# Kernel tuning notes

Hardware: AMD Instinct MI355X
Metric: run time of the kernel (lower is better)

Reference implementation:

```python
import jax, jax.numpy as jnp
import numpy as np

B, T, D = 4, 2048, 768
H = 12
DH = D // H
DFF = 3072
EPS = 1e-5


def _layernorm(x, g, b):
    mu = jnp.mean(x, axis=-1, keepdims=True)
    var = jnp.var(x, axis=-1, keepdims=True)
    return (x - mu) * jax.lax.rsqrt(var + EPS) * g + b


def setup_inputs() -> dict:
    key = jax.random.key(0)
    ks = jax.random.split(key, 12)
    s = lambda fan_in: 1.0 / np.sqrt(fan_in)
    return {
        "x": jax.random.normal(ks[0], (B, T, D), dtype=jnp.float32),
        "ln1_g": jnp.ones((D,), jnp.float32),
        "ln1_b": jnp.zeros((D,), jnp.float32),
        "w_qkv": jax.random.uniform(ks[1], (D, 3 * D), jnp.float32, -s(D), s(D)),
        "b_qkv": jax.random.uniform(ks[2], (3 * D,), jnp.float32, -s(D), s(D)),
        "w_proj": jax.random.uniform(ks[3], (D, D), jnp.float32, -s(D), s(D)),
        "b_proj": jax.random.uniform(ks[4], (D,), jnp.float32, -s(D), s(D)),
        "ln2_g": jnp.ones((D,), jnp.float32),
        "ln2_b": jnp.zeros((D,), jnp.float32),
        "w_ff1": jax.random.uniform(ks[5], (D, DFF), jnp.float32, -s(D), s(D)),
        "b_ff1": jax.random.uniform(ks[6], (DFF,), jnp.float32, -s(D), s(D)),
        "w_ff2": jax.random.uniform(ks[7], (DFF, D), jnp.float32, -s(DFF), s(DFF)),
        "b_ff2": jax.random.uniform(ks[8], (D,), jnp.float32, -s(DFF), s(DFF)),
    }


def reference(x, ln1_g, ln1_b, w_qkv, b_qkv, w_proj, b_proj,
              ln2_g, ln2_b, w_ff1, b_ff1, w_ff2, b_ff2):
    # --- attention sublayer ---
    h = _layernorm(x, ln1_g, ln1_b)
    qkv = h @ w_qkv + b_qkv                       # [B,T,3D]
    q, k, v = jnp.split(qkv, 3, axis=-1)
    q = q.reshape(B, T, H, DH).transpose(0, 2, 1, 3)  # [B,H,T,DH]
    k = k.reshape(B, T, H, DH).transpose(0, 2, 1, 3)
    v = v.reshape(B, T, H, DH).transpose(0, 2, 1, 3)
    att = jnp.einsum('bhqd,bhkd->bhqk', q, k) / jnp.sqrt(jnp.float32(DH))
    causal = jnp.tril(jnp.ones((T, T), dtype=bool))
    att = jnp.where(causal, att, -jnp.inf)
    att = jax.nn.softmax(att, axis=-1)
    out = jnp.einsum('bhqk,bhkd->bhqd', att, v)    # [B,H,T,DH]
    out = out.transpose(0, 2, 1, 3).reshape(B, T, D)
    x = x + out @ w_proj + b_proj
    # --- MLP sublayer ---
    h2 = _layernorm(x, ln2_g, ln2_b)
    h2 = jax.nn.gelu(h2 @ w_ff1 + b_ff1, approximate=False)
    x = x + h2 @ w_ff2 + b_ff2
    return x
```

## Files before the change

### kernel.cpp

```cpp
#include <hip/hip_runtime.h>
#include <cstdint>
#include <cstddef>

typedef unsigned short u16;
typedef unsigned int u32;
typedef __attribute__((ext_vector_type(8))) short s16x8;
typedef __attribute__((ext_vector_type(4))) float f32x4;

#define NB 4
#define NT 2048
#define ND 768
#define NH 12
#define NDH 64
#define NFF 3072
#define NM (NB*NT)

__device__ __forceinline__ u16 f2b(float f){
  union { float f; unsigned u; } c; c.f = f;
  unsigned r = c.u + 0x7fffu + ((c.u >> 16) & 1u);
  return (u16)(r >> 16);
}

__device__ __forceinline__ f32x4 mfma16(s16x8 a, s16x8 b, f32x4 c){
  return __builtin_amdgcn_mfma_f32_16x16x32_bf16(a, b, c, 0, 0, 0);
}

__device__ __forceinline__ void stage16(u16* lds, const u16* g){
  __builtin_amdgcn_global_load_lds(
      (const __attribute__((address_space(1))) unsigned int*)g,
      (__attribute__((address_space(3))) unsigned int*)lds,
      16, 0, 0);
}

__global__ __launch_bounds__(256) void transpose_bf16(
    const float* __restrict__ in, u16* __restrict__ out, int K, int N)
{
  __shared__ float tile[32][33];
  const int n0 = blockIdx.x * 32, k0 = blockIdx.y * 32;
  const int tx = threadIdx.x, ty = threadIdx.y;
  #pragma unroll
  for (int i = 0; i < 32; i += 8)
    tile[ty + i][tx] = in[(size_t)(k0 + ty + i) * N + n0 + tx];
  __syncthreads();
  #pragma unroll
  for (int i = 0; i < 32; i += 8)
    out[(size_t)(n0 + ty + i) * K + k0 + tx] = f2b(tile[tx][ty + i]);
}

__global__ __launch_bounds__(256) void ln_kernel(
    const float* __restrict__ x, const float* __restrict__ g,
    const float* __restrict__ b, u16* __restrict__ out)
{
  const int row = blockIdx.x;
  const int t = threadIdx.x;
  const float* xr = x + (size_t)row * ND;
  float v0 = xr[t], v1 = xr[t + 256], v2 = xr[t + 512];
  float s = v0 + v1 + v2;
  float ss = v0*v0 + v1*v1 + v2*v2;
  #pragma unroll
  for (int o = 32; o; o >>= 1) { s += __shfl_xor(s, o, 64); ss += __shfl_xor(ss, o, 64); }
  __shared__ float red[8];
  const int w = t >> 6;
  if ((t & 63) == 0) { red[w] = s; red[4 + w] = ss; }
  __syncthreads();
  s  = red[0] + red[1] + red[2] + red[3];
  ss = red[4] + red[5] + red[6] + red[7];
  const float mu = s * (1.f / ND);
  const float var = ss * (1.f / ND) - mu * mu;
  const float rinv = rsqrtf(var + 1e-5f);
  u16* orow = out + (size_t)row * ND;
  orow[t]       = f2b((v0 - mu) * rinv * g[t]       + b[t]);
  orow[t + 256] = f2b((v1 - mu) * rinv * g[t + 256] + b[t + 256]);
  orow[t + 512] = f2b((v2 - mu) * rinv * g[t + 512] + b[t + 512]);
}

template<int EPI>
__global__ __launch_bounds__(256,4) void gemm_bt(
    const u16* __restrict__ A, const u16* __restrict__ Bt,
    const float* __restrict__ bias, const float* __restrict__ res,
    void* __restrict__ o0, void* __restrict__ o1, void* __restrict__ o2,
    const int M, const int N, const int K)
{
  __shared__ u16 As[128 * 32];
  __shared__ u16 Bs[128 * 32];
  const int tid = threadIdx.x;
  const int lane = tid & 63, wid = tid >> 6;
  const int wr = wid >> 1, wc = wid & 1;
  const int lg = lane >> 4, lm = lane & 15;
  const int bm = blockIdx.x * 128, bn = blockIdx.y * 128;

  f32x4 acc[4][4] = {};

  const u16* ApT = A  + (size_t)(bm + (tid >> 2)) * K + (tid & 3) * 8;
  const u16* BpT = Bt + (size_t)(bn + (tid >> 2)) * K + (tid & 3) * 8;
  u16* AsW = &As[wid * 512];
  u16* BsW = &Bs[wid * 512];
  const size_t rowStride64 = (size_t)64 * K;

  for (int k0 = 0; k0 < K; k0 += 32) {
    __syncthreads();
    stage16(AsW,        ApT + k0);
    stage16(AsW + 2048, ApT + rowStride64 + k0);
    stage16(BsW,        BpT + k0);
    stage16(BsW + 2048, BpT + rowStride64 + k0);
    __syncthreads();
    s16x8 af[4], bf[4];
    #pragma unroll
    for (int i = 0; i < 4; i++) af[i] = *(const s16x8*)&As[(wr * 64 + i * 16 + lm) * 32 + lg * 8];
    #pragma unroll
    for (int j = 0; j < 4; j++) bf[j] = *(const s16x8*)&Bs[(wc * 64 + j * 16 + lm) * 32 + lg * 8];
    #pragma unroll
    for (int i = 0; i < 4; i++)
      #pragma unroll
      for (int j = 0; j < 4; j++)
        acc[i][j] = mfma16(af[i], bf[j], acc[i][j]);
  }

  #pragma unroll
  for (int i = 0; i < 4; i++)
    #pragma unroll
    for (int j = 0; j < 4; j++) {
      const int col = bn + wc * 64 + j * 16 + lm;
      const float bb = bias[col];
      #pragma unroll
      for (int r = 0; r < 4; r++) {
        const int row = bm + wr * 64 + i * 16 + lg * 4 + r;
        float v = acc[i][j][r] + bb;
        if (EPI == 0) {
          u16* dst; int rem;
          if (col < ND)            { dst = (u16*)o0; rem = col; v *= 0.125f; }
          else if (col < 2 * ND)   { dst = (u16*)o1; rem = col - ND; }
          else                     { dst = (u16*)o2; rem = col - 2 * ND; }
          const int hh = rem >> 6, dh = rem & 63;
          const int bb2 = row >> 11, tt = row & 2047;
          dst[(((size_t)bb2 * NH + hh) * NT + tt) * NDH + dh] = f2b(v);
        } else if (EPI == 1) {
          ((float*)o0)[(size_t)row * ND + col] = v + res[(size_t)row * ND + col];
        } else if (EPI == 2) {
          const float ge = 0.5f * v * (1.f + erff(v * 0.70710678118654752f));
          ((u16*)o0)[(size_t)row * NFF + col] = f2b(ge);
        } else {
          ((float*)o0)[(size_t)row * ND + col] = v + res[(size_t)row * ND + col];
        }
      }
    }
}

__global__ __launch_bounds__(256,2) void attn_kernel(
    const u16* __restrict__ Q, const u16* __restrict__ Kg,
    const u16* __restrict__ V, u16* __restrict__ O)
{
  const int pairIdx = blockIdx.x;
  const int bh = blockIdx.y;
  const int b = bh / NH, h = bh % NH;
  const int tid = threadIdx.x;
  const int lane = tid & 63, w = tid >> 6;
  const int lg = lane >> 4, lm = lane & 15;
  const int sr = tid >> 3;
  const int sc = (tid & 7) * 8;

  __shared__ u16 Ks[64 * 64];
  __shared__ u16 Vt[64 * 64];
  __shared__ u16 Ps[4][16 * 64];

  const u16* Qb = Q  + (size_t)bh * NT * NDH;
  const u16* Kb = Kg + (size_t)bh * NT * NDH;
  const u16* Vb = V  + (size_t)bh * NT * NDH;

  for (int half = 0; half < 2; ++half) {
    const int si = half ? (31 - pairIdx) : pairIdx;
    const int q0 = si * 64;
    const int ktmax = si;

    const s16x8 qf0 = *(const s16x8*)&Qb[(size_t)(q0 + w * 16 + lm) * NDH + lg * 8];
    const s16x8 qf1 = *(const s16x8*)&Qb[(size_t)(q0 + w * 16 + lm) * NDH + 32 + lg * 8];

    f32x4 oacc[4] = {};
    float m = -INFINITY, l = 0.f;

    s16x8 kva = *(const s16x8*)&Kb[(size_t)sr * NDH + sc];
    s16x8 kvb = *(const s16x8*)&Kb[(size_t)(sr + 32) * NDH + sc];
    s16x8 vva = *(const s16x8*)&Vb[(size_t)sr * NDH + sc];
    s16x8 vvb = *(const s16x8*)&Vb[(size_t)(sr + 32) * NDH + sc];

    for (int kt = 0; kt <= ktmax; ++kt) {
      __syncthreads();
      *(s16x8*)&Ks[sr * 64 + (sc ^ ((sr & 7) << 3))] = kva;
      *(s16x8*)&Ks[(sr + 32) * 64 + (sc ^ ((sr & 7) << 3))] = kvb;
      #pragma unroll
      for (int e = 0; e < 8; ++e)
        Vt[(sc + e) * 64 + (sr ^ ((tid & 7) << 3))] = (u16)vva[e];
      #pragma unroll
      for (int e = 0; e < 8; ++e)
        Vt[(sc + e) * 64 + ((sr + 32) ^ ((tid & 7) << 3))] = (u16)vvb[e];
      __syncthreads();

      if (kt < ktmax) {
        const u16* Kn = Kb + (size_t)(kt + 1) * 64 * NDH;
        const u16* Vn = Vb + (size_t)(kt + 1) * 64 * NDH;
        kva = *(const s16x8*)&Kn[(size_t)sr * NDH + sc];
        kvb = *(const s16x8*)&Kn[(size_t)(sr + 32) * NDH + sc];
        vva = *(const s16x8*)&Vn[(size_t)sr * NDH + sc];
        vvb = *(const s16x8*)&Vn[(size_t)(sr + 32) * NDH + sc];
      }

      f32x4 sv[4];
      #pragma unroll
      for (int n = 0; n < 4; ++n) {
        const int krow = (n * 16 + lm) * 64;
        const int swz = (lm & 7) << 3;
        s16x8 kf0 = *(const s16x8*)&Ks[krow + ((lg * 8) ^ swz)];
        s16x8 kf1 = *(const s16x8*)&Ks[krow + ((32 + lg * 8) ^ swz)];
        f32x4 s4 = {};
        s4 = mfma16(kf0, qf0, s4);
        s4 = mfma16(kf1, qf1, s4);
        sv[n] = s4;
      }

      if (kt == ktmax) {
        #pragma unroll
        for (int n = 0; n < 4; ++n)
          #pragma unroll
          for (int r = 0; r < 4; ++r)
            if (n * 16 + lg * 4 + r > w * 16 + lm) sv[n][r] = -INFINITY;
      }

      float mx = -INFINITY;
      #pragma unroll
      for (int n = 0; n < 4; ++n)
        #pragma unroll
        for (int r = 0; r < 4; ++r) mx = fmaxf(mx, sv[n][r]);
      mx = fmaxf(mx, __shfl_xor(mx, 16));
      mx = fmaxf(mx, __shfl_xor(mx, 32));
      const float mnew = fmaxf(m, mx);
      const float alpha = __expf(m - mnew);
      m = mnew;

      float rs = 0.f;
      u32 pk[4][2];
      #pragma unroll
      for (int n = 0; n < 4; ++n) {
        const float p0 = __expf(sv[n][0] - mnew);
        const float p1 = __expf(sv[n][1] - mnew);
        const float p2 = __expf(sv[n][2] - mnew);
        const float p3 = __expf(sv[n][3] - mnew);
        rs += (p0 + p1) + (p2 + p3);
        pk[n][0] = (u32)f2b(p0) | ((u32)f2b(p1) << 16);
        pk[n][1] = (u32)f2b(p2) | ((u32)f2b(p3) << 16);
      }
      rs += __shfl_xor(rs, 16);
      rs += __shfl_xor(rs, 32);
      l = l * alpha + rs;

      #pragma unroll
      for (int n = 0; n < 4; ++n) {
        const int idx0 = lm * 64 + ((n * 16 + lg * 4) ^ ((lm & 7) << 3));
        *(u32*)&Ps[w][idx0] = pk[n][0];
        *(u32*)&Ps[w][idx0 + 2] = pk[n][1];
      }

      float av[4];
      #pragma unroll
      for (int r = 0; r < 4; ++r) av[r] = __shfl(alpha, lg * 4 + r);
      #pragma unroll
      for (int d = 0; d < 4; ++d)
        #pragma unroll
        for (int r = 0; r < 4; ++r) oacc[d][r] *= av[r];

      #pragma unroll
      for (int kh = 0; kh < 2; ++kh) {
        const s16x8 pf = *(const s16x8*)&Ps[w][lm * 64 + ((kh * 32 + lg * 8) ^ ((lm & 7) << 3))];
        #pragma unroll
        for (int dt = 0; dt < 4; ++dt) {
          const int g = (2 * dt + (lm >> 3)) & 7;
          const s16x8 vf = *(const s16x8*)&Vt[(dt * 16 + lm) * 64 + (((kh * 4 + lg) ^ g) << 3)];
          oacc[dt] = mfma16(pf, vf, oacc[dt]);
        }
      }
    }

    float lv[4];
    #pragma unroll
    for (int r = 0; r < 4; ++r) lv[r] = 1.f / __shfl(l, lg * 4 + r);
    #pragma unroll
    for (int dt = 0; dt < 4; ++dt)
      #pragma unroll
      for (int r = 0; r < 4; ++r) {
        const int qg = q0 + w * 16 + lg * 4 + r;
        O[((size_t)b * NT + qg) * ND + h * NDH + dt * 16 + lm] = f2b(oacc[dt][r] * lv[r]);
      }
  }
}

extern "C" void kernel_launch(void* const* d_in, const int* in_sizes, int n_in,
                              void* d_out, int out_size, void* d_ws, size_t ws_size,
                              hipStream_t stream)
{
  const float* x      = (const float*)d_in[0];
  const float* ln1_g  = (const float*)d_in[1];
  const float* ln1_b  = (const float*)d_in[2];
  const float* w_qkv  = (const float*)d_in[3];
  const float* b_qkv  = (const float*)d_in[4];
  const float* w_proj = (const float*)d_in[5];
  const float* b_proj = (const float*)d_in[6];
  const float* ln2_g  = (const float*)d_in[7];
  const float* ln2_b  = (const float*)d_in[8];
  const float* w_ff1  = (const float*)d_in[9];
  const float* b_ff1  = (const float*)d_in[10];
  const float* w_ff2  = (const float*)d_in[11];
  const float* b_ff2  = (const float*)d_in[12];

  char* ws = (char*)d_ws;
  u16*   wt_qkv = (u16*)(ws + 0);
  u16*   wt_proj= (u16*)(ws + 3538944);
  u16*   wt_ff1 = (u16*)(ws + 4718592);
  u16*   wt_ff2 = (u16*)(ws + 9437184);
  u16*   hbuf   = (u16*)(ws + 14155776);
  u16*   qbuf   = (u16*)(ws + 26738688);
  u16*   kbuf   = (u16*)(ws + 39321600);
  u16*   vbuf   = (u16*)(ws + 51904512);
  u16*   aobuf  = (u16*)(ws + 64487424);
  float* x1     = (float*)(ws + 77070336);
  u16*   h2buf  = (u16*)(ws + 102236160);
  u16*   ff1buf = hbuf;

  transpose_bf16<<<dim3(2304/32,  768/32), dim3(32,8), 0, stream>>>(w_qkv,  wt_qkv,  768, 2304);
  transpose_bf16<<<dim3( 768/32,  768/32), dim3(32,8), 0, stream>>>(w_proj, wt_proj, 768,  768);
  transpose_bf16<<<dim3(3072/32,  768/32), dim3(32,8), 0, stream>>>(w_ff1,  wt_ff1,  768, 3072);
  transpose_bf16<<<dim3( 768/32, 3072/32), dim3(32,8), 0, stream>>>(w_ff2,  wt_ff2, 3072,  768);

  ln_kernel<<<NM, 256, 0, stream>>>(x, ln1_g, ln1_b, hbuf);
  gemm_bt<0><<<dim3(NM/128, 2304/128), 256, 0, stream>>>(hbuf, wt_qkv, b_qkv, nullptr,
                                                         qbuf, kbuf, vbuf, NM, 2304, ND);
  attn_kernel<<<dim3(16, NB*NH), 256, 0, stream>>>(qbuf, kbuf, vbuf, aobuf);
  gemm_bt<1><<<dim3(NM/128, ND/128), 256, 0, stream>>>(aobuf, wt_proj, b_proj, x,
                                                       x1, nullptr, nullptr, NM, ND, ND);
  ln_kernel<<<NM, 256, 0, stream>>>(x1, ln2_g, ln2_b, h2buf);
  gemm_bt<2><<<dim3(NM/128, NFF/128), 256, 0, stream>>>(h2buf, wt_ff1, b_ff1, nullptr,
                                                        ff1buf, nullptr, nullptr, NM, NFF, ND);
  gemm_bt<3><<<dim3(NM/128, ND/128), 256, 0, stream>>>(ff1buf, wt_ff2, b_ff2, x1,
                                                       d_out, nullptr, nullptr, NM, ND, NFF);
}
```

Measured before the change: 305.1 us.

## Use 512-thread GEMM blocks with XOR LDS swizzle, block remap and fast GELU

The GEMM now runs 8 waves per 128x128 tile, each wave owning a 32x64 sub-tile, so each thread issues one A and one B staging load per K step instead of two. An XOR swizzle on the staged chunk and on the fragment reads is meant to cut LDS bank conflicts. Block IDs are remapped across groups of 8, apparently to spread neighbouring tiles across XCDs for cache locality. The exact erf in the FF1 epilogue is replaced with the Abramowitz-Stegun polynomial plus exp, which is cheaper but only accurate to about 1e-7 absolute.

```diff
diff --git a/kernel.cpp b/kernel.cpp
--- a/kernel.cpp
+++ b/kernel.cpp
@@ -30,6 +30,17 @@
       (const __attribute__((address_space(1))) unsigned int*)g,
       (__attribute__((address_space(3))) unsigned int*)lds,
       16, 0, 0);
+}
+
+__device__ __forceinline__ float gelu_f(float v){
+  const float x = v * 0.70710678118654752f;
+  const float ax = fabsf(x);
+  const float t = 1.f / (1.f + 0.3275911f * ax);
+  const float y = t * (0.254829592f + t * (-0.284496736f + t * (1.421413741f
+                + t * (-1.453152027f + t * 1.061405429f))));
+  float er = 1.f - y * __expf(-ax * ax);
+  er = copysignf(er, x);
+  return 0.5f * v * (1.f + er);
 }
 
 __global__ __launch_bounds__(256) void transpose_bf16(
@@ -75,7 +86,7 @@
 }
 
 template<int EPI>
-__global__ __launch_bounds__(256,4) void gemm_bt(
+__global__ __launch_bounds__(512,6) void gemm_bt(
     const u16* __restrict__ A, const u16* __restrict__ Bt,
     const float* __restrict__ bias, const float* __restrict__ res,
     void* __restrict__ o0, void* __restrict__ o1, void* __restrict__ o2,
@@ -87,44 +98,51 @@
   const int lane = tid & 63, wid = tid >> 6;
   const int wr = wid >> 1, wc = wid & 1;
   const int lg = lane >> 4, lm = lane & 15;
-  const int bm = blockIdx.x * 128, bn = blockIdx.y * 128;
-
-  f32x4 acc[4][4] = {};
-
-  const u16* ApT = A  + (size_t)(bm + (tid >> 2)) * K + (tid & 3) * 8;
-  const u16* BpT = Bt + (size_t)(bn + (tid >> 2)) * K + (tid & 3) * 8;
-  u16* AsW = &As[wid * 512];
-  u16* BsW = &Bs[wid * 512];
-  const size_t rowStride64 = (size_t)64 * K;
-
-  for (int k0 = 0; k0 < K; k0 += 32) {
+
+  const int nwg = gridDim.x * gridDim.y;
+  int bid = blockIdx.y * gridDim.x + blockIdx.x;
+  bid = (bid & 7) * (nwg >> 3) + (bid >> 3);
+  const int bm = (bid & 63) * 128, bn = (bid >> 6) * 128;
+
+  f32x4 acc[2][4] = {};
+
+  const int srow = tid >> 2;
+  const int schunk = (tid & 3) ^ ((tid >> 3) & 3);
+  const u16* ApT = A  + (size_t)(bm + srow) * K + schunk * 8;
+  const u16* BpT = Bt + (size_t)(bn + srow) * K + schunk * 8;
+  const int woff = wid * 512;
+  const int fswz = (lm >> 1) & 3;
+
+  const int nt = K >> 5;
+  for (int t = 0; t < nt; ++t) {
+    const int k0 = t << 5;
     __syncthreads();
-    stage16(AsW,        ApT + k0);
-    stage16(AsW + 2048, ApT + rowStride64 + k0);
-    stage16(BsW,        BpT + k0);
-    stage16(BsW + 2048, BpT + rowStride64 + k0);
+    stage16(&As[woff], ApT + k0);
+    stage16(&Bs[woff], BpT + k0);
     __syncthreads();
-    s16x8 af[4], bf[4];
-    #pragma unroll
-    for (int i = 0; i < 4; i++) af[i] = *(const s16x8*)&As[(wr * 64 + i * 16 + lm) * 32 + lg * 8];
-    #pragma unroll
-    for (int j = 0; j < 4; j++) bf[j] = *(const s16x8*)&Bs[(wc * 64 + j * 16 + lm) * 32 + lg * 8];
-    #pragma unroll
-    for (int i = 0; i < 4; i++)
+    s16x8 af[2], bf[4];
+    #pragma unroll
+    for (int i = 0; i < 2; i++)
+      af[i] = *(const s16x8*)&As[(wr * 32 + i * 16 + lm) * 32 + ((lg ^ fswz) * 8)];
+    #pragma unroll
+    for (int j = 0; j < 4; j++)
+      bf[j] = *(const s16x8*)&Bs[(wc * 64 + j * 16 + lm) * 32 + ((lg ^ fswz) * 8)];
+    #pragma unroll
+    for (int i = 0; i < 2; i++)
       #pragma unroll
       for (int j = 0; j < 4; j++)
         acc[i][j] = mfma16(af[i], bf[j], acc[i][j]);
   }
 
   #pragma unroll
-  for (int i = 0; i < 4; i++)
+  for (int i = 0; i < 2; i++)
     #pragma unroll
     for (int j = 0; j < 4; j++) {
       const int col = bn + wc * 64 + j * 16 + lm;
       const float bb = bias[col];
       #pragma unroll
       for (int r = 0; r < 4; r++) {
-        const int row = bm + wr * 64 + i * 16 + lg * 4 + r;
+        const int row = bm + wr * 32 + i * 16 + lg * 4 + r;
         float v = acc[i][j][r] + bb;
         if (EPI == 0) {
           u16* dst; int rem;
@@ -137,8 +155,7 @@
         } else if (EPI == 1) {
           ((float*)o0)[(size_t)row * ND + col] = v + res[(size_t)row * ND + col];
         } else if (EPI == 2) {
-          const float ge = 0.5f * v * (1.f + erff(v * 0.70710678118654752f));
-          ((u16*)o0)[(size_t)row * NFF + col] = f2b(ge);
+          ((u16*)o0)[(size_t)row * NFF + col] = f2b(gelu_f(v));
         } else {
           ((float*)o0)[(size_t)row * ND + col] = v + res[(size_t)row * ND + col];
         }
@@ -330,14 +347,14 @@
   transpose_bf16<<<dim3( 768/32, 3072/32), dim3(32,8), 0, stream>>>(w_ff2,  wt_ff2, 3072,  768);
 
   ln_kernel<<<NM, 256, 0, stream>>>(x, ln1_g, ln1_b, hbuf);
-  gemm_bt<0><<<dim3(NM/128, 2304/128), 256, 0, stream>>>(hbuf, wt_qkv, b_qkv, nullptr,
+  gemm_bt<0><<<dim3(NM/128, 2304/128), 512, 0, stream>>>(hbuf, wt_qkv, b_qkv, nullptr,
                                                          qbuf, kbuf, vbuf, NM, 2304, ND);
   attn_kernel<<<dim3(16, NB*NH), 256, 0, stream>>>(qbuf, kbuf, vbuf, aobuf);
-  gemm_bt<1><<<dim3(NM/128, ND/128), 256, 0, stream>>>(aobuf, wt_proj, b_proj, x,
+  gemm_bt<1><<<dim3(NM/128, ND/128), 512, 0, stream>>>(aobuf, wt_proj, b_proj, x,
                                                        x1, nullptr, nullptr, NM, ND, ND);
   ln_kernel<<<NM, 256, 0, stream>>>(x1, ln2_g, ln2_b, h2buf);
-  gemm_bt<2><<<dim3(NM/128, NFF/128), 256, 0, stream>>>(h2buf, wt_ff1, b_ff1, nullptr,
+  gemm_bt<2><<<dim3(NM/128, NFF/128), 512, 0, stream>>>(h2buf, wt_ff1, b_ff1, nullptr,
                                                         ff1buf, nullptr, nullptr, NM, NFF, ND);
-  gemm_bt<3><<<dim3(NM/128, ND/128), 256, 0, stream>>>(ff1buf, wt_ff2, b_ff2, x1,
+  gemm_bt<3><<<dim3(NM/128, ND/128), 512, 0, stream>>>(ff1buf, wt_ff2, b_ff2, x1,
                                                        d_out, nullptr, nullptr, NM, ND, NFF);
 }
```

Measured after the change: 328.5 us. +7.7%, slower.
